# Kernel tuning notes

Measured on AMD Instinct MI355X. Metric: run time of the kernel, lower is better.

The kernel has to match this reference:

```python
import jax, jax.numpy as jnp
from jax import lax
import numpy as np

V, E, H, L = 512, 512, 1024, 2
B, T = 128, 512
PAD = 0


def _uniform(k, shape, bound):
    return jax.random.uniform(k, shape, jnp.float32, -bound, bound)


def setup_inputs() -> dict:
    key = jax.random.key(0)
    ks = jax.random.split(key, 14)
    kH = 1.0 / np.sqrt(H)
    inp = {
        'seq': jax.random.randint(ks[0], (B, T), 0, V, dtype=jnp.int32),
        'seq_lens': jax.random.randint(ks[1], (B,), 1, T + 1, dtype=jnp.int32),
        'teacher_p': jnp.asarray(0.5, jnp.float32),
        'embeds': jax.random.normal(ks[2], (V, E), jnp.float32),
        # layer 0: input size E; layer 1: input size H (PyTorch gate order i,f,g,o)
        'W_ih0': _uniform(ks[3], (4 * H, E), kH),
        'W_hh0': _uniform(ks[4], (4 * H, H), kH),
        'b_ih0': _uniform(ks[5], (4 * H,), kH),
        'b_hh0': _uniform(ks[6], (4 * H,), kH),
        'W_ih1': _uniform(ks[7], (4 * H, H), kH),
        'W_hh1': _uniform(ks[8], (4 * H, H), kH),
        'b_ih1': _uniform(ks[9], (4 * H,), kH),
        'b_hh1': _uniform(ks[10], (4 * H,), kH),
        'fc_w': _uniform(ks[11], (V, H), 1.0 / np.sqrt(H)),
        'fc_b': _uniform(ks[12], (V,), 1.0 / np.sqrt(H)),
    }
    return inp


def _lstm_cell(x, h, c, Wih, Whh, bih, bhh):
    g = x @ Wih.T + h @ Whh.T + (bih + bhh)  # [B, 4H]
    i, f, gg, o = jnp.split(g, 4, axis=-1)
    c = jax.nn.sigmoid(f) * c + jax.nn.sigmoid(i) * jnp.tanh(gg)
    h = jax.nn.sigmoid(o) * jnp.tanh(c)
    return h, c


def reference(seq, seq_lens, teacher_p, embeds, W_ih0, W_hh0, b_ih0, b_hh0,
              W_ih1, W_hh1, b_ih1, b_hh1, fc_w, fc_b):
    emb = embeds.at[PAD].set(0.0)  # padding_idx row is zero
    # pre-drawn teacher-forcing uniforms, one per (t, b)
    u = jax.random.uniform(jax.random.key(1), (T, B), jnp.float32)

    def step(carry, xs):
        h0, c0, h1, c1, prev_logits = carry
        tok_t, u_t, t = xs
        use_teacher = (t == 0) | (u_t < teacher_p)
        tok = jnp.where(use_teacher, tok_t, jnp.argmax(prev_logits, axis=1).astype(tok_t.dtype))
        x = emb[tok]  # [B, E]
        h0, c0 = _lstm_cell(x, h0, c0, W_ih0, W_hh0, b_ih0, b_hh0)
        h1, c1 = _lstm_cell(h0, h1, c1, W_ih1, W_hh1, b_ih1, b_hh1)
        logits = h1 @ fc_w.T + fc_b  # [B, V]
        return (h0, c0, h1, c1, logits), logits

    z = jnp.zeros((B, H), jnp.float32)
    init = (z, z, z, z, jnp.zeros((B, V), jnp.float32))
    xs = (seq.T, u, jnp.arange(T))
    _, logits = lax.scan(step, init, xs)  # [T, B, V]
    return jnp.transpose(logits, (1, 0, 2))  # [B, T, V]
```

## Files before the change

### kernel.cpp

```cpp
#include <hip/hip_runtime.h>
#include <cstdint>
#include <cstddef>

#define BB 128
#define TT 512
#define VV 512
#define EE 512
#define HH 1024
#define G4H 4096
#define KC 256

__device__ __forceinline__ float tf_uniform(unsigned i) {
  unsigned x0 = 0u;
  unsigned x1 = i;
  const unsigned k0 = 0u, k1 = 1u, k2 = 0x1BD11BDBu;
  x0 += k0; x1 += k1;
#define ROTL_(v, r) (((v) << (r)) | ((v) >> (32 - (r))))
#define RND_(r) { x0 += x1; x1 = ROTL_(x1, (r)); x1 ^= x0; }
  RND_(13) RND_(15) RND_(26) RND_(6)   x0 += k1; x1 += k2 + 1u;
  RND_(17) RND_(29) RND_(16) RND_(24)  x0 += k2; x1 += k0 + 2u;
  RND_(13) RND_(15) RND_(26) RND_(6)   x0 += k0; x1 += k1 + 3u;
  RND_(17) RND_(29) RND_(16) RND_(24)  x0 += k1; x1 += k2 + 4u;
  RND_(13) RND_(15) RND_(26) RND_(6)   x0 += k2; x1 += k0 + 5u;
#undef RND_
#undef ROTL_
  unsigned bits = x0 ^ x1;
  unsigned fb = (bits >> 9) | 0x3f800000u;
  return __uint_as_float(fb) - 1.0f;
}

__global__ __launch_bounds__(256) void init_kernel(float* __restrict__ h0a,
                                                   float* __restrict__ c0,
                                                   float* __restrict__ h1a,
                                                   float* __restrict__ c1) {
  int tid = blockIdx.x * 256 + threadIdx.x;
  if (tid < BB * HH) {
    h0a[tid] = 0.f; c0[tid] = 0.f; h1a[tid] = 0.f; c1[tid] = 0.f;
  }
}

__global__ __launch_bounds__(256) void gates_kernel(
    const float* __restrict__ A1, int nc1, int ld1, const float* __restrict__ W1,
    const float* __restrict__ A2, int ld2, const float* __restrict__ W2,
    int gather1,
    const float* __restrict__ emb,
    const int* __restrict__ seq,
    const float* __restrict__ teacher_p,
    const unsigned long long* __restrict__ fcpart,
    int t,
    float* __restrict__ gpart) {
  __shared__ float Xs[32][132];
  __shared__ float Ws[32][132];
  __shared__ int tok_s[BB];

  const int tid = threadIdx.x;
  const int s = blockIdx.y;
  const int n0 = blockIdx.x * 128;

  const float* A; const float* W; int ldk, koff, gath;
  if (s < nc1) { A = A1; W = W1; ldk = ld1; koff = s * KC; gath = gather1; }
  else         { A = A2; W = W2; ldk = ld2; koff = (s - nc1) * KC; gath = 0; }

  if (gath) {
    if (tid < BB) {
      int sel;
      if (t == 0) {
        sel = seq[(size_t)tid * TT];
      } else {
        float uu = tf_uniform((unsigned)(t * BB + tid));
        if (uu < teacher_p[0]) {
          sel = seq[(size_t)tid * TT + t];
        } else {
          const unsigned long long* fp = fcpart + (size_t)tid * 32;
          unsigned long long best = fp[0];
#pragma unroll 8
          for (int j = 1; j < 32; ++j) {
            unsigned long long k2 = fp[j];
            if (k2 > best) best = k2;
          }
          sel = (int)(0xFFFFFFFFu - (unsigned)(best & 0xFFFFFFFFull));
        }
      }
      tok_s[tid] = sel;
    }
    __syncthreads();
  }

  const int ty = tid >> 4;
  const int tx = tid & 15;

  float acc[8][8];
#pragma unroll
  for (int i = 0; i < 8; ++i)
#pragma unroll
    for (int jj = 0; jj < 8; ++jj) acc[i][jj] = 0.f;

  for (int kt = 0; kt < 8; ++kt) {
#pragma unroll
    for (int i = 0; i < 4; ++i) {
      int f = tid + i * 256;
      int row = f >> 3;
      int kq = f & 7;
      int kg = koff + kt * 32 + kq * 4;
      float4 v;
      if (gath) {
        int tk = tok_s[row];
        if (tk == 0) v = make_float4(0.f, 0.f, 0.f, 0.f);
        else v = *(const float4*)(emb + (size_t)tk * ldk + kg);
      } else {
        v = *(const float4*)(A + (size_t)row * ldk + kg);
      }
      int kk = kq * 4;
      Xs[kk + 0][row] = v.x; Xs[kk + 1][row] = v.y;
      Xs[kk + 2][row] = v.z; Xs[kk + 3][row] = v.w;
      float4 w = *(const float4*)(W + (size_t)(n0 + row) * ldk + kg);
      Ws[kk + 0][row] = w.x; Ws[kk + 1][row] = w.y;
      Ws[kk + 2][row] = w.z; Ws[kk + 3][row] = w.w;
    }
    __syncthreads();
#pragma unroll 8
    for (int k = 0; k < 32; ++k) {
      float a[8], bb[8];
      *(float4*)&a[0] = *(const float4*)&Xs[k][ty * 4];
      *(float4*)&a[4] = *(const float4*)&Xs[k][64 + ty * 4];
      *(float4*)&bb[0] = *(const float4*)&Ws[k][tx * 4];
      *(float4*)&bb[4] = *(const float4*)&Ws[k][64 + tx * 4];
#pragma unroll
      for (int i = 0; i < 8; ++i)
#pragma unroll
        for (int jj = 0; jj < 8; ++jj)
          acc[i][jj] = fmaf(a[i], bb[jj], acc[i][jj]);
    }
    __syncthreads();
  }

  float* gp = gpart + (size_t)s * BB * G4H;
#pragma unroll
  for (int ih = 0; ih < 2; ++ih) {
#pragma unroll
    for (int i = 0; i < 4; ++i) {
      int b = ih * 64 + ty * 4 + i;
      int ai = ih * 4 + i;
      float* dst = gp + (size_t)b * G4H + n0;
      *(float4*)(dst + tx * 4) =
          make_float4(acc[ai][0], acc[ai][1], acc[ai][2], acc[ai][3]);
      *(float4*)(dst + 64 + tx * 4) =
          make_float4(acc[ai][4], acc[ai][5], acc[ai][6], acc[ai][7]);
    }
  }
}

__global__ __launch_bounds__(256) void cell_kernel(
    const float* __restrict__ gpart, int S,
    const float* __restrict__ bih, const float* __restrict__ bhh,
    float* __restrict__ c, float* __restrict__ h_out) {
  int tid = blockIdx.x * 256 + threadIdx.x;
  int b = tid >> 10;
  int u = tid & 1023;
  float gi = bih[u] + bhh[u];
  float gf = bih[HH + u] + bhh[HH + u];
  float gg = bih[2 * HH + u] + bhh[2 * HH + u];
  float go = bih[3 * HH + u] + bhh[3 * HH + u];
  for (int s = 0; s < S; ++s) {
    const float* gp = gpart + ((size_t)(s * BB + b)) * G4H + u;
    gi += gp[0];
    gf += gp[HH];
    gg += gp[2 * HH];
    go += gp[3 * HH];
  }
  float i_ = 1.f / (1.f + expf(-gi));
  float f_ = 1.f / (1.f + expf(-gf));
  float g_ = tanhf(gg);
  float o_ = 1.f / (1.f + expf(-go));
  float cn = f_ * c[tid] + i_ * g_;
  c[tid] = cn;
  h_out[tid] = o_ * tanhf(cn);
}

__global__ __launch_bounds__(256) void fc_kernel(
    const float* __restrict__ h1,
    const float* __restrict__ fcw, const float* __restrict__ fcb,
    float* __restrict__ out, unsigned long long* __restrict__ fcpart, int t) {
  __shared__ float Xs[32][132];
  __shared__ float Wsh[32][20];
  const int tid = threadIdx.x;
  const int n0 = blockIdx.x * 16;
  const int tb = tid >> 3;
  const int tn = tid & 7;
  float acc[4][2] = {{0.f, 0.f}, {0.f, 0.f}, {0.f, 0.f}, {0.f, 0.f}};

  for (int kt = 0; kt < 32; ++kt) {
#pragma unroll
    for (int i = 0; i < 4; ++i) {
      int f = tid + i * 256;
      int row = f >> 3, kq = f & 7;
      float4 v = *(const float4*)(h1 + (size_t)row * HH + kt * 32 + kq * 4);
      int kk = kq * 4;
      Xs[kk + 0][row] = v.x; Xs[kk + 1][row] = v.y;
      Xs[kk + 2][row] = v.z; Xs[kk + 3][row] = v.w;
    }
    if (tid < 128) {
      int row = tid >> 3, kq = tid & 7;
      float4 v = *(const float4*)(fcw + (size_t)(n0 + row) * HH + kt * 32 + kq * 4);
      int kk = kq * 4;
      Wsh[kk + 0][row] = v.x; Wsh[kk + 1][row] = v.y;
      Wsh[kk + 2][row] = v.z; Wsh[kk + 3][row] = v.w;
    }
    __syncthreads();
#pragma unroll 8
    for (int k = 0; k < 32; ++k) {
      float4 a = *(const float4*)&Xs[k][tb * 4];
      float b0 = Wsh[k][tn * 2], b1 = Wsh[k][tn * 2 + 1];
      acc[0][0] = fmaf(a.x, b0, acc[0][0]); acc[0][1] = fmaf(a.x, b1, acc[0][1]);
      acc[1][0] = fmaf(a.y, b0, acc[1][0]); acc[1][1] = fmaf(a.y, b1, acc[1][1]);
      acc[2][0] = fmaf(a.z, b0, acc[2][0]); acc[2][1] = fmaf(a.z, b1, acc[2][1]);
      acc[3][0] = fmaf(a.w, b0, acc[3][0]); acc[3][1] = fmaf(a.w, b1, acc[3][1]);
    }
    __syncthreads();
  }

#pragma unroll
  for (int i = 0; i < 4; ++i) {
    int b = tb * 4 + i;
    unsigned long long key = 0ull;
#pragma unroll
    for (int jj = 0; jj < 2; ++jj) {
      int n = n0 + tn * 2 + jj;
      float lg = acc[i][jj] + fcb[n];
      out[((size_t)b * TT + t) * VV + n] = lg;
      unsigned sbits = __float_as_uint(lg);
      sbits = (sbits & 0x80000000u) ? ~sbits : (sbits | 0x80000000u);
      unsigned long long kk =
          ((unsigned long long)sbits << 32) |
          (unsigned long long)(0xFFFFFFFFu - (unsigned)n);
      if (kk > key) key = kk;
    }
#pragma unroll
    for (int off = 4; off > 0; off >>= 1) {
      unsigned long long o = __shfl_down(key, off, 8);
      if (o > key) key = o;
    }
    if (tn == 0) fcpart[(size_t)b * 32 + blockIdx.x] = key;
  }
}

extern "C" void kernel_launch(void* const* d_in, const int* in_sizes, int n_in,
                              void* d_out, int out_size, void* d_ws, size_t ws_size,
                              hipStream_t stream) {
  const int*   seq       = (const int*)d_in[0];
  const float* teacher_p = (const float*)d_in[2];
  const float* embeds    = (const float*)d_in[3];
  const float* W_ih0     = (const float*)d_in[4];
  const float* W_hh0     = (const float*)d_in[5];
  const float* b_ih0     = (const float*)d_in[6];
  const float* b_hh0     = (const float*)d_in[7];
  const float* W_ih1     = (const float*)d_in[8];
  const float* W_hh1     = (const float*)d_in[9];
  const float* b_ih1     = (const float*)d_in[10];
  const float* b_hh1     = (const float*)d_in[11];
  const float* fc_w      = (const float*)d_in[12];
  const float* fc_b      = (const float*)d_in[13];
  float* out = (float*)d_out;

  char* ws = (char*)d_ws;
  const size_t BH = (size_t)BB * HH;
  float* h0    = (float*)(ws);
  float* c0    = (float*)(ws + 2 * BH * 4);
  float* h1    = (float*)(ws + 3 * BH * 4);
  float* c1    = (float*)(ws + 5 * BH * 4);
  unsigned long long* fcpart = (unsigned long long*)(ws + 6 * BH * 4);
  float* gpart = (float*)(ws + 6 * BH * 4 + 65536);

  init_kernel<<<512, 256, 0, stream>>>(h0, c0, h1, c1);

  for (int t = 0; t < TT; ++t) {
    float* h0r = h0 + (size_t)(t & 1) * BH;
    float* h0w = h0 + (size_t)((t + 1) & 1) * BH;
    float* h1r = h1 + (size_t)(t & 1) * BH;
    float* h1w = h1 + (size_t)((t + 1) & 1) * BH;

    gates_kernel<<<dim3(32, 6), 256, 0, stream>>>(
        nullptr, 2, EE, W_ih0, h0r, HH, W_hh0, 1,
        embeds, seq, teacher_p, fcpart, t, gpart);
    cell_kernel<<<512, 256, 0, stream>>>(gpart, 6, b_ih0, b_hh0, c0, h0w);

    gates_kernel<<<dim3(32, 8), 256, 0, stream>>>(
        h0w, 4, HH, W_ih1, h1r, HH, W_hh1, 0,
        embeds, seq, teacher_p, fcpart, t, gpart);
    cell_kernel<<<512, 256, 0, stream>>>(gpart, 8, b_ih1, b_hh1, c1, h1w);

    fc_kernel<<<32, 256, 0, stream>>>(h1w, fc_w, fc_b, out, fcpart, t);
  }
}
```

Before: 90.44 ms.

## Replace per-step kernel launches with one persistent cooperative kernel using grid barriers

Replaces the five launches per timestep (gates, cell and fc kernels) with a single persistent cooperative kernel of 256 blocks. Each block owns 4 hidden units across all four gates, so the gate GEMM and the cell update are fused and the split-K partial buffer goes away. Hidden and cell state are stored transposed, loads are register-prefetched, and steps are separated by atomic grid barriers. This removes launch overhead and partial-sum round trips through global memory. In exchange it adds three grid barriers per step and gives each block a small tile with low arithmetic intensity.

```diff
diff --git a/kernel.cpp b/kernel.cpp
--- a/kernel.cpp
+++ b/kernel.cpp
@@ -7,8 +7,8 @@
 #define VV 512
 #define EE 512
 #define HH 1024
-#define G4H 4096
-#define KC 256
+#define NBLK 256
+#define BHS ((size_t)BB * HH)
 
 __device__ __forceinline__ float tf_uniform(unsigned i) {
   unsigned x0 = 0u;
@@ -29,218 +29,327 @@
   return __uint_as_float(fb) - 1.0f;
 }
 
-__global__ __launch_bounds__(256) void init_kernel(float* __restrict__ h0a,
-                                                   float* __restrict__ c0,
-                                                   float* __restrict__ h1a,
-                                                   float* __restrict__ c1) {
+__device__ __forceinline__ void gridbar(unsigned* bar, unsigned target) {
+  __syncthreads();
+  if (threadIdx.x == 0) {
+    __threadfence();
+    __hip_atomic_fetch_add(bar, 1u, __ATOMIC_RELAXED, __HIP_MEMORY_SCOPE_AGENT);
+    while (__hip_atomic_fetch_add(bar, 0u, __ATOMIC_RELAXED, __HIP_MEMORY_SCOPE_AGENT) < target) {
+      __builtin_amdgcn_s_sleep(1);
+    }
+    __threadfence();
+  }
+  __syncthreads();
+}
+
+__global__ __launch_bounds__(256) void init_kernel(float* __restrict__ h0T,
+                                                   float* __restrict__ c0T,
+                                                   float* __restrict__ h1T,
+                                                   float* __restrict__ c1T,
+                                                   unsigned* __restrict__ bar) {
   int tid = blockIdx.x * 256 + threadIdx.x;
-  if (tid < BB * HH) {
-    h0a[tid] = 0.f; c0[tid] = 0.f; h1a[tid] = 0.f; c1[tid] = 0.f;
+  if (tid == 0) *bar = 0u;
+  if (tid < (int)BHS) {
+    h0T[tid] = 0.f; c0T[tid] = 0.f; h1T[tid] = 0.f; c1T[tid] = 0.f;
   }
 }
 
-__global__ __launch_bounds__(256) void gates_kernel(
-    const float* __restrict__ A1, int nc1, int ld1, const float* __restrict__ W1,
-    const float* __restrict__ A2, int ld2, const float* __restrict__ W2,
-    int gather1,
-    const float* __restrict__ emb,
+__global__ __launch_bounds__(256, 1) void lstm_persistent(
     const int* __restrict__ seq,
     const float* __restrict__ teacher_p,
-    const unsigned long long* __restrict__ fcpart,
-    int t,
-    float* __restrict__ gpart) {
+    const float* __restrict__ emb,
+    const float* __restrict__ Wih0, const float* __restrict__ Whh0,
+    const float* __restrict__ bih0, const float* __restrict__ bhh0,
+    const float* __restrict__ Wih1, const float* __restrict__ Whh1,
+    const float* __restrict__ bih1, const float* __restrict__ bhh1,
+    const float* __restrict__ fcw, const float* __restrict__ fcb,
+    float* __restrict__ out,
+    float* __restrict__ h0T, float* __restrict__ c0T,
+    float* __restrict__ h1T, float* __restrict__ c1T,
+    unsigned long long* __restrict__ fcpart,
+    unsigned* __restrict__ bar) {
   __shared__ float Xs[32][132];
-  __shared__ float Ws[32][132];
+  __shared__ float Ws2[16][36];
+  __shared__ float Xsf[64][36];
+  __shared__ float Wsf[8][68];
   __shared__ int tok_s[BB];
 
   const int tid = threadIdx.x;
-  const int s = blockIdx.y;
-  const int n0 = blockIdx.x * 128;
-
-  const float* A; const float* W; int ldk, koff, gath;
-  if (s < nc1) { A = A1; W = W1; ldk = ld1; koff = s * KC; gath = gather1; }
-  else         { A = A2; W = W2; ldk = ld2; koff = (s - nc1) * KC; gath = 0; }
-
-  if (gath) {
-    if (tid < BB) {
-      int sel;
-      if (t == 0) {
-        sel = seq[(size_t)tid * TT];
-      } else {
-        float uu = tf_uniform((unsigned)(t * BB + tid));
-        if (uu < teacher_p[0]) {
-          sel = seq[(size_t)tid * TT + t];
+  const int bn  = blockIdx.x;
+  const int ty  = tid >> 3;
+  const int tx  = tid & 7;
+
+  const float tp = teacher_p[0];
+
+  float bc0[2][4], bc1[2][4];
+#pragma unroll
+  for (int r = 0; r < 2; ++r) {
+    int j = (tid + (r << 8)) >> 7;
+    int u = (bn << 2) + j;
+#pragma unroll
+    for (int g = 0; g < 4; ++g) {
+      bc0[r][g] = bih0[g * HH + u] + bhh0[g * HH + u];
+      bc1[r][g] = bih1[g * HH + u] + bhh1[g * HH + u];
+    }
+  }
+
+  const int wc  = tid >> 3;
+  const int wkq = tid & 7;
+  const int gr  = (wc >> 2) * HH + (bn << 2) + (wc & 3);
+  const float* wih0row = Wih0 + (size_t)gr * EE;
+  const float* whh0row = Whh0 + (size_t)gr * HH;
+  const float* wih1row = Wih1 + (size_t)gr * HH;
+  const float* whh1row = Whh1 + (size_t)gr * HH;
+
+  const int rb = bn >> 6, cb = bn & 63;
+  const int fb = tid >> 3;
+  const int fcc = tid & 7;
+  const int fn = (cb << 3) + fcc;
+  const float fcbr = fcb[fn];
+  const float* fcwrow = fcw + (size_t)((cb << 3) + (tid >> 4)) * HH;
+
+  unsigned target = 0;
+
+  for (int t = 0; t < TT; ++t) {
+    const float* h0r = h0T + (size_t)(t & 1) * BHS;
+    float*       h0w = h0T + (size_t)((t + 1) & 1) * BHS;
+    const float* h1r = h1T + (size_t)(t & 1) * BHS;
+    float*       h1w = h1T + (size_t)((t + 1) & 1) * BHS;
+
+    {
+      int b = tid >> 1, h = tid & 1;
+      unsigned long long best = 0ull;
+      if (t > 0) {
+        const unsigned long long* fp = fcpart + ((size_t)b << 6);
+#pragma unroll 8
+        for (int i = 0; i < 32; ++i) {
+          unsigned long long k2 = fp[(i << 1) + h];
+          if (k2 > best) best = k2;
+        }
+        unsigned long long o = __shfl_xor(best, 1);
+        if (o > best) best = o;
+      }
+      if (h == 0) {
+        int sel;
+        if (t == 0) {
+          sel = seq[(size_t)b * TT];
         } else {
-          const unsigned long long* fp = fcpart + (size_t)tid * 32;
-          unsigned long long best = fp[0];
-#pragma unroll 8
-          for (int j = 1; j < 32; ++j) {
-            unsigned long long k2 = fp[j];
-            if (k2 > best) best = k2;
+          float uu = tf_uniform((unsigned)(t * BB + b));
+          sel = (uu < tp) ? seq[(size_t)b * TT + t]
+                          : (int)(0xFFFFFFFFu - (unsigned)(best & 0xFFFFFFFFull));
+        }
+        tok_s[b] = sel;
+      }
+    }
+    __syncthreads();
+
+    {
+      float acc[4][2] = {{0.f,0.f},{0.f,0.f},{0.f,0.f},{0.f,0.f}};
+      float4 x0, x1, x2, x3, w;
+
+      auto pf = [&](int kt) {
+        if (kt < 16) {
+          const int kb = kt << 5;
+          { int f=tid;     int b=f>>3, kq=f&7; int tk=tok_s[b];
+            x0 = tk ? *(const float4*)(emb + ((size_t)tk<<9) + kb + (kq<<2)) : make_float4(0.f,0.f,0.f,0.f); }
+          { int f=tid+256; int b=f>>3, kq=f&7; int tk=tok_s[b];
+            x1 = tk ? *(const float4*)(emb + ((size_t)tk<<9) + kb + (kq<<2)) : make_float4(0.f,0.f,0.f,0.f); }
+          { int f=tid+512; int b=f>>3, kq=f&7; int tk=tok_s[b];
+            x2 = tk ? *(const float4*)(emb + ((size_t)tk<<9) + kb + (kq<<2)) : make_float4(0.f,0.f,0.f,0.f); }
+          { int f=tid+768; int b=f>>3, kq=f&7; int tk=tok_s[b];
+            x3 = tk ? *(const float4*)(emb + ((size_t)tk<<9) + kb + (kq<<2)) : make_float4(0.f,0.f,0.f,0.f); }
+          if (tid < 128) w = *(const float4*)(wih0row + kb + (wkq<<2));
+        } else {
+          const float* src = h0r + ((size_t)(kt - 16) << 5) * BB;
+          { int f=tid;     x0 = *(const float4*)(src + (f>>5)*BB + ((f&31)<<2)); }
+          { int f=tid+256; x1 = *(const float4*)(src + (f>>5)*BB + ((f&31)<<2)); }
+          { int f=tid+512; x2 = *(const float4*)(src + (f>>5)*BB + ((f&31)<<2)); }
+          { int f=tid+768; x3 = *(const float4*)(src + (f>>5)*BB + ((f&31)<<2)); }
+          if (tid < 128) w = *(const float4*)(whh0row + ((kt - 16) << 5) + (wkq<<2));
+        }
+      };
+      auto st = [&](int kt) {
+        if (kt < 16) {
+          { int f=tid;     int b=f>>3, kk=(f&7)<<2; Xs[kk][b]=x0.x; Xs[kk+1][b]=x0.y; Xs[kk+2][b]=x0.z; Xs[kk+3][b]=x0.w; }
+          { int f=tid+256; int b=f>>3, kk=(f&7)<<2; Xs[kk][b]=x1.x; Xs[kk+1][b]=x1.y; Xs[kk+2][b]=x1.z; Xs[kk+3][b]=x1.w; }
+          { int f=tid+512; int b=f>>3, kk=(f&7)<<2; Xs[kk][b]=x2.x; Xs[kk+1][b]=x2.y; Xs[kk+2][b]=x2.z; Xs[kk+3][b]=x2.w; }
+          { int f=tid+768; int b=f>>3, kk=(f&7)<<2; Xs[kk][b]=x3.x; Xs[kk+1][b]=x3.y; Xs[kk+2][b]=x3.z; Xs[kk+3][b]=x3.w; }
+        } else {
+          { int f=tid;     *(float4*)&Xs[f>>5][(f&31)<<2] = x0; }
+          { int f=tid+256; *(float4*)&Xs[f>>5][(f&31)<<2] = x1; }
+          { int f=tid+512; *(float4*)&Xs[f>>5][(f&31)<<2] = x2; }
+          { int f=tid+768; *(float4*)&Xs[f>>5][(f&31)<<2] = x3; }
+        }
+        if (tid < 128) *(float4*)&Ws2[wc][wkq<<2] = w;
+      };
+
+      pf(0);
+      for (int kt = 0; kt < 48; ++kt) {
+        st(kt);
+        __syncthreads();
+        if (kt < 47) pf(kt + 1);
+#pragma unroll
+        for (int k4 = 0; k4 < 8; ++k4) {
+          float w0[4], w1[4];
+          *(float4*)w0 = *(const float4*)&Ws2[tx << 1][k4 << 2];
+          *(float4*)w1 = *(const float4*)&Ws2[(tx << 1) + 1][k4 << 2];
+#pragma unroll
+          for (int kk = 0; kk < 4; ++kk) {
+            float a[4];
+            *(float4*)a = *(const float4*)&Xs[(k4 << 2) + kk][ty << 2];
+#pragma unroll
+            for (int i = 0; i < 4; ++i) {
+              acc[i][0] = fmaf(a[i], w0[kk], acc[i][0]);
+              acc[i][1] = fmaf(a[i], w1[kk], acc[i][1]);
+            }
           }
-          sel = (int)(0xFFFFFFFFu - (unsigned)(best & 0xFFFFFFFFull));
-        }
-      }
-      tok_s[tid] = sel;
-    }
-    __syncthreads();
-  }
-
-  const int ty = tid >> 4;
-  const int tx = tid & 15;
-
-  float acc[8][8];
-#pragma unroll
-  for (int i = 0; i < 8; ++i)
-#pragma unroll
-    for (int jj = 0; jj < 8; ++jj) acc[i][jj] = 0.f;
-
-  for (int kt = 0; kt < 8; ++kt) {
-#pragma unroll
-    for (int i = 0; i < 4; ++i) {
-      int f = tid + i * 256;
-      int row = f >> 3;
-      int kq = f & 7;
-      int kg = koff + kt * 32 + kq * 4;
-      float4 v;
-      if (gath) {
-        int tk = tok_s[row];
-        if (tk == 0) v = make_float4(0.f, 0.f, 0.f, 0.f);
-        else v = *(const float4*)(emb + (size_t)tk * ldk + kg);
-      } else {
-        v = *(const float4*)(A + (size_t)row * ldk + kg);
-      }
-      int kk = kq * 4;
-      Xs[kk + 0][row] = v.x; Xs[kk + 1][row] = v.y;
-      Xs[kk + 2][row] = v.z; Xs[kk + 3][row] = v.w;
-      float4 w = *(const float4*)(W + (size_t)(n0 + row) * ldk + kg);
-      Ws[kk + 0][row] = w.x; Ws[kk + 1][row] = w.y;
-      Ws[kk + 2][row] = w.z; Ws[kk + 3][row] = w.w;
-    }
-    __syncthreads();
-#pragma unroll 8
-    for (int k = 0; k < 32; ++k) {
-      float a[8], bb[8];
-      *(float4*)&a[0] = *(const float4*)&Xs[k][ty * 4];
-      *(float4*)&a[4] = *(const float4*)&Xs[k][64 + ty * 4];
-      *(float4*)&bb[0] = *(const float4*)&Ws[k][tx * 4];
-      *(float4*)&bb[4] = *(const float4*)&Ws[k][64 + tx * 4];
-#pragma unroll
-      for (int i = 0; i < 8; ++i)
-#pragma unroll
-        for (int jj = 0; jj < 8; ++jj)
-          acc[i][jj] = fmaf(a[i], bb[jj], acc[i][jj]);
-    }
-    __syncthreads();
-  }
-
-  float* gp = gpart + (size_t)s * BB * G4H;
-#pragma unroll
-  for (int ih = 0; ih < 2; ++ih) {
-#pragma unroll
-    for (int i = 0; i < 4; ++i) {
-      int b = ih * 64 + ty * 4 + i;
-      int ai = ih * 4 + i;
-      float* dst = gp + (size_t)b * G4H + n0;
-      *(float4*)(dst + tx * 4) =
-          make_float4(acc[ai][0], acc[ai][1], acc[ai][2], acc[ai][3]);
-      *(float4*)(dst + 64 + tx * 4) =
-          make_float4(acc[ai][4], acc[ai][5], acc[ai][6], acc[ai][7]);
-    }
-  }
-}
-
-__global__ __launch_bounds__(256) void cell_kernel(
-    const float* __restrict__ gpart, int S,
-    const float* __restrict__ bih, const float* __restrict__ bhh,
-    float* __restrict__ c, float* __restrict__ h_out) {
-  int tid = blockIdx.x * 256 + threadIdx.x;
-  int b = tid >> 10;
-  int u = tid & 1023;
-  float gi = bih[u] + bhh[u];
-  float gf = bih[HH + u] + bhh[HH + u];
-  float gg = bih[2 * HH + u] + bhh[2 * HH + u];
-  float go = bih[3 * HH + u] + bhh[3 * HH + u];
-  for (int s = 0; s < S; ++s) {
-    const float* gp = gpart + ((size_t)(s * BB + b)) * G4H + u;
-    gi += gp[0];
-    gf += gp[HH];
-    gg += gp[2 * HH];
-    go += gp[3 * HH];
-  }
-  float i_ = 1.f / (1.f + expf(-gi));
-  float f_ = 1.f / (1.f + expf(-gf));
-  float g_ = tanhf(gg);
-  float o_ = 1.f / (1.f + expf(-go));
-  float cn = f_ * c[tid] + i_ * g_;
-  c[tid] = cn;
-  h_out[tid] = o_ * tanhf(cn);
-}
-
-__global__ __launch_bounds__(256) void fc_kernel(
-    const float* __restrict__ h1,
-    const float* __restrict__ fcw, const float* __restrict__ fcb,
-    float* __restrict__ out, unsigned long long* __restrict__ fcpart, int t) {
-  __shared__ float Xs[32][132];
-  __shared__ float Wsh[32][20];
-  const int tid = threadIdx.x;
-  const int n0 = blockIdx.x * 16;
-  const int tb = tid >> 3;
-  const int tn = tid & 7;
-  float acc[4][2] = {{0.f, 0.f}, {0.f, 0.f}, {0.f, 0.f}, {0.f, 0.f}};
-
-  for (int kt = 0; kt < 32; ++kt) {
-#pragma unroll
-    for (int i = 0; i < 4; ++i) {
-      int f = tid + i * 256;
-      int row = f >> 3, kq = f & 7;
-      float4 v = *(const float4*)(h1 + (size_t)row * HH + kt * 32 + kq * 4);
-      int kk = kq * 4;
-      Xs[kk + 0][row] = v.x; Xs[kk + 1][row] = v.y;
-      Xs[kk + 2][row] = v.z; Xs[kk + 3][row] = v.w;
-    }
-    if (tid < 128) {
-      int row = tid >> 3, kq = tid & 7;
-      float4 v = *(const float4*)(fcw + (size_t)(n0 + row) * HH + kt * 32 + kq * 4);
-      int kk = kq * 4;
-      Wsh[kk + 0][row] = v.x; Wsh[kk + 1][row] = v.y;
-      Wsh[kk + 2][row] = v.z; Wsh[kk + 3][row] = v.w;
-    }
-    __syncthreads();
-#pragma unroll 8
-    for (int k = 0; k < 32; ++k) {
-      float4 a = *(const float4*)&Xs[k][tb * 4];
-      float b0 = Wsh[k][tn * 2], b1 = Wsh[k][tn * 2 + 1];
-      acc[0][0] = fmaf(a.x, b0, acc[0][0]); acc[0][1] = fmaf(a.x, b1, acc[0][1]);
-      acc[1][0] = fmaf(a.y, b0, acc[1][0]); acc[1][1] = fmaf(a.y, b1, acc[1][1]);
-      acc[2][0] = fmaf(a.z, b0, acc[2][0]); acc[2][1] = fmaf(a.z, b1, acc[2][1]);
-      acc[3][0] = fmaf(a.w, b0, acc[3][0]); acc[3][1] = fmaf(a.w, b1, acc[3][1]);
-    }
-    __syncthreads();
-  }
-
-#pragma unroll
-  for (int i = 0; i < 4; ++i) {
-    int b = tb * 4 + i;
-    unsigned long long key = 0ull;
-#pragma unroll
-    for (int jj = 0; jj < 2; ++jj) {
-      int n = n0 + tn * 2 + jj;
-      float lg = acc[i][jj] + fcb[n];
-      out[((size_t)b * TT + t) * VV + n] = lg;
+        }
+        __syncthreads();
+      }
+
+      float* gbuf = &Xs[0][0];
+#pragma unroll
+      for (int i = 0; i < 4; ++i) {
+        int r = (ty << 2) + i;
+        gbuf[r * 17 + (tx << 1)]     = acc[i][0];
+        gbuf[r * 17 + (tx << 1) + 1] = acc[i][1];
+      }
+      __syncthreads();
+#pragma unroll
+      for (int r = 0; r < 2; ++r) {
+        int idx = tid + (r << 8);
+        int b = idx & 127, j = idx >> 7;
+        float gi = gbuf[b * 17 + j]      + bc0[r][0];
+        float gf = gbuf[b * 17 + 4 + j]  + bc0[r][1];
+        float gg = gbuf[b * 17 + 8 + j]  + bc0[r][2];
+        float go = gbuf[b * 17 + 12 + j] + bc0[r][3];
+        float i_ = 1.f / (1.f + expf(-gi));
+        float f_ = 1.f / (1.f + expf(-gf));
+        float g_ = tanhf(gg);
+        float o_ = 1.f / (1.f + expf(-go));
+        size_t off = ((size_t)((bn << 2) + j)) * BB + b;
+        float cn = f_ * c0T[off] + i_ * g_;
+        c0T[off] = cn;
+        h0w[off] = o_ * tanhf(cn);
+      }
+    }
+    target += NBLK; gridbar(bar, target);
+
+    {
+      float acc[4][2] = {{0.f,0.f},{0.f,0.f},{0.f,0.f},{0.f,0.f}};
+      float4 x0, x1, x2, x3, w;
+
+      auto pf2 = [&](int kt) {
+        const float* src = (kt < 32) ? (h0w + ((size_t)kt << 5) * BB)
+                                     : (h1r + ((size_t)(kt - 32) << 5) * BB);
+        { int f=tid;     x0 = *(const float4*)(src + (f>>5)*BB + ((f&31)<<2)); }
+        { int f=tid+256; x1 = *(const float4*)(src + (f>>5)*BB + ((f&31)<<2)); }
+        { int f=tid+512; x2 = *(const float4*)(src + (f>>5)*BB + ((f&31)<<2)); }
+        { int f=tid+768; x3 = *(const float4*)(src + (f>>5)*BB + ((f&31)<<2)); }
+        if (tid < 128) {
+          w = (kt < 32) ? *(const float4*)(wih1row + (kt << 5) + (wkq<<2))
+                        : *(const float4*)(whh1row + ((kt - 32) << 5) + (wkq<<2));
+        }
+      };
+      auto st2 = [&]() {
+        { int f=tid;     *(float4*)&Xs[f>>5][(f&31)<<2] = x0; }
+        { int f=tid+256; *(float4*)&Xs[f>>5][(f&31)<<2] = x1; }
+        { int f=tid+512; *(float4*)&Xs[f>>5][(f&31)<<2] = x2; }
+        { int f=tid+768; *(float4*)&Xs[f>>5][(f&31)<<2] = x3; }
+        if (tid < 128) *(float4*)&Ws2[wc][wkq<<2] = w;
+      };
+
+      pf2(0);
+      for (int kt = 0; kt < 64; ++kt) {
+        st2();
+        __syncthreads();
+        if (kt < 63) pf2(kt + 1);
+#pragma unroll
+        for (int k4 = 0; k4 < 8; ++k4) {
+          float w0[4], w1[4];
+          *(float4*)w0 = *(const float4*)&Ws2[tx << 1][k4 << 2];
+          *(float4*)w1 = *(const float4*)&Ws2[(tx << 1) + 1][k4 << 2];
+#pragma unroll
+          for (int kk = 0; kk < 4; ++kk) {
+            float a[4];
+            *(float4*)a = *(const float4*)&Xs[(k4 << 2) + kk][ty << 2];
+#pragma unroll
+            for (int i = 0; i < 4; ++i) {
+              acc[i][0] = fmaf(a[i], w0[kk], acc[i][0]);
+              acc[i][1] = fmaf(a[i], w1[kk], acc[i][1]);
+            }
+          }
+        }
+        __syncthreads();
+      }
+
+      float* gbuf = &Xs[0][0];
+#pragma unroll
+      for (int i = 0; i < 4; ++i) {
+        int r = (ty << 2) + i;
+        gbuf[r * 17 + (tx << 1)]     = acc[i][0];
+        gbuf[r * 17 + (tx << 1) + 1] = acc[i][1];
+      }
+      __syncthreads();
+#pragma unroll
+      for (int r = 0; r < 2; ++r) {
+        int idx = tid + (r << 8);
+        int b = idx & 127, j = idx >> 7;
+        float gi = gbuf[b * 17 + j]      + bc1[r][0];
+        float gf = gbuf[b * 17 + 4 + j]  + bc1[r][1];
+        float gg = gbuf[b * 17 + 8 + j]  + bc1[r][2];
+        float go = gbuf[b * 17 + 12 + j] + bc1[r][3];
+        float i_ = 1.f / (1.f + expf(-gi));
+        float f_ = 1.f / (1.f + expf(-gf));
+        float g_ = tanhf(gg);
+        float o_ = 1.f / (1.f + expf(-go));
+        size_t off = ((size_t)((bn << 2) + j)) * BB + b;
+        float cn = f_ * c1T[off] + i_ * g_;
+        c1T[off] = cn;
+        h1w[off] = o_ * tanhf(cn);
+      }
+    }
+    target += NBLK; gridbar(bar, target);
+
+    {
+      float facc = 0.f;
+      float4 y0, y1, fw;
+      auto pf3 = [&](int kt) {
+        const float* src = h1w + ((size_t)kt << 6) * BB + ((size_t)rb << 5);
+        { int f=tid;     y0 = *(const float4*)(src + (f>>3)*BB + ((f&7)<<2)); }
+        { int f=tid+256; y1 = *(const float4*)(src + (f>>3)*BB + ((f&7)<<2)); }
+        if (tid < 128) fw = *(const float4*)(fcwrow + (kt << 6) + ((tid & 15) << 2));
+      };
+      auto st3 = [&]() {
+        { int f=tid;     *(float4*)&Xsf[f>>3][(f&7)<<2] = y0; }
+        { int f=tid+256; *(float4*)&Xsf[f>>3][(f&7)<<2] = y1; }
+        if (tid < 128) *(float4*)&Wsf[tid >> 4][(tid & 15) << 2] = fw;
+      };
+      pf3(0);
+      for (int kt = 0; kt < 16; ++kt) {
+        st3();
+        __syncthreads();
+        if (kt < 15) pf3(kt + 1);
+#pragma unroll
+        for (int k = 0; k < 64; ++k)
+          facc = fmaf(Xsf[k][fb], Wsf[fcc][k], facc);
+        __syncthreads();
+      }
+      int b = (rb << 5) + fb;
+      float lg = facc + fcbr;
+      out[((size_t)b * TT + t) * VV + fn] = lg;
       unsigned sbits = __float_as_uint(lg);
       sbits = (sbits & 0x80000000u) ? ~sbits : (sbits | 0x80000000u);
-      unsigned long long kk =
-          ((unsigned long long)sbits << 32) |
-          (unsigned long long)(0xFFFFFFFFu - (unsigned)n);
-      if (kk > key) key = kk;
-    }
-#pragma unroll
-    for (int off = 4; off > 0; off >>= 1) {
-      unsigned long long o = __shfl_down(key, off, 8);
-      if (o > key) key = o;
-    }
-    if (tn == 0) fcpart[(size_t)b * 32 + blockIdx.x] = key;
+      unsigned long long key = ((unsigned long long)sbits << 32) |
+                               (unsigned long long)(0xFFFFFFFFu - (unsigned)fn);
+#pragma unroll
+      for (int off = 4; off > 0; off >>= 1) {
+        unsigned long long o = __shfl_down(key, off, 8);
+        if (o > key) key = o;
+      }
+      if (fcc == 0) fcpart[((size_t)b << 6) + cb] = key;
+    }
+    target += NBLK; gridbar(bar, target);
   }
 }
 
@@ -263,32 +372,29 @@
   float* out = (float*)d_out;
 
   char* ws = (char*)d_ws;
-  const size_t BH = (size_t)BB * HH;
-  float* h0    = (float*)(ws);
-  float* c0    = (float*)(ws + 2 * BH * 4);
-  float* h1    = (float*)(ws + 3 * BH * 4);
-  float* c1    = (float*)(ws + 5 * BH * 4);
-  unsigned long long* fcpart = (unsigned long long*)(ws + 6 * BH * 4);
-  float* gpart = (float*)(ws + 6 * BH * 4 + 65536);
-
-  init_kernel<<<512, 256, 0, stream>>>(h0, c0, h1, c1);
-
-  for (int t = 0; t < TT; ++t) {
-    float* h0r = h0 + (size_t)(t & 1) * BH;
-    float* h0w = h0 + (size_t)((t + 1) & 1) * BH;
-    float* h1r = h1 + (size_t)(t & 1) * BH;
-    float* h1w = h1 + (size_t)((t + 1) & 1) * BH;
-
-    gates_kernel<<<dim3(32, 6), 256, 0, stream>>>(
-        nullptr, 2, EE, W_ih0, h0r, HH, W_hh0, 1,
-        embeds, seq, teacher_p, fcpart, t, gpart);
-    cell_kernel<<<512, 256, 0, stream>>>(gpart, 6, b_ih0, b_hh0, c0, h0w);
-
-    gates_kernel<<<dim3(32, 8), 256, 0, stream>>>(
-        h0w, 4, HH, W_ih1, h1r, HH, W_hh1, 0,
-        embeds, seq, teacher_p, fcpart, t, gpart);
-    cell_kernel<<<512, 256, 0, stream>>>(gpart, 8, b_ih1, b_hh1, c1, h1w);
-
-    fc_kernel<<<32, 256, 0, stream>>>(h1w, fc_w, fc_b, out, fcpart, t);
+  float* h0T = (float*)(ws);
+  float* c0T = (float*)(ws + 2 * BHS * 4);
+  float* h1T = (float*)(ws + 3 * BHS * 4);
+  float* c1T = (float*)(ws + 5 * BHS * 4);
+  unsigned long long* fcpart = (unsigned long long*)(ws + 6 * BHS * 4);
+  unsigned* bar = (unsigned*)(ws + 6 * BHS * 4 + 65536);
+
+  init_kernel<<<512, 256, 0, stream>>>(h0T, c0T, h1T, c1T, bar);
+
+  void* args[] = {
+    (void*)&seq, (void*)&teacher_p, (void*)&embeds,
+    (void*)&W_ih0, (void*)&W_hh0, (void*)&b_ih0, (void*)&b_hh0,
+    (void*)&W_ih1, (void*)&W_hh1, (void*)&b_ih1, (void*)&b_hh1,
+    (void*)&fc_w, (void*)&fc_b, (void*)&out,
+    (void*)&h0T, (void*)&c0T, (void*)&h1T, (void*)&c1T,
+    (void*)&fcpart, (void*)&bar
+  };
+  hipError_t err = hipLaunchCooperativeKernel((void*)lstm_persistent,
+                                              dim3(NBLK), dim3(256), args, 0, stream);
+  if (err != hipSuccess) {
+    lstm_persistent<<<dim3(NBLK), dim3(256), 0, stream>>>(
+        seq, teacher_p, embeds, W_ih0, W_hh0, b_ih0, b_hh0,
+        W_ih1, W_hh1, b_ih1, b_hh1, fc_w, fc_b, out,
+        h0T, c0T, h1T, c1T, fcpart, bar);
   }
 }
```

After: 108.1 ms. 1.2x slower.
